# Performance work log

Measured on AMD Instinct MI355X. Metric: run time of the kernel, lower is better.

The kernel has to match this reference:

```python
import jax, jax.numpy as jnp
import numpy as np

H = 12      # num_attention_heads
D = 768     # hidden_size
DK = D // H # per-head dim


def setup_inputs() -> dict:
    key = jax.random.key(0)
    ks = jax.random.split(key, 8)
    B, S = 2, 4096
    scale = 0.02
    return {
        "query": jax.random.normal(ks[0], (B, S, D), jnp.float32),
        "key": jax.random.normal(ks[1], (B, S, D), jnp.float32),
        "value": jax.random.normal(ks[2], (B, S, D), jnp.float32),
        "mask": jnp.ones((B, S), jnp.float32),
        "Wq": jax.random.normal(ks[3], (D, D), jnp.float32) * scale,
        "bq": jnp.zeros((D,), jnp.float32),
        "Wk": jax.random.normal(ks[4], (D, D), jnp.float32) * scale,
        "bk": jnp.zeros((D,), jnp.float32),
        "Wv": jax.random.normal(ks[5], (D, D), jnp.float32) * scale,
        "bv": jnp.zeros((D,), jnp.float32),
    }


def reference(query, key, value, mask, Wq, bq, Wk, bk, Wv, bv):
    B, Sq, _ = query.shape
    Sk = key.shape[1]
    # attention mask: ones[B,Sq,1] * mask[B,1,Sk] -> [B,Sq,Sk] -> [B,1,Sq,Sk]
    attn_mask = jnp.ones((B, Sq, 1), jnp.float32) * mask[:, None, :]
    adder = (1.0 - attn_mask)[:, None, :, :] * -10000.0

    q = (query @ Wq + bq).reshape(B, Sq, H, DK).transpose(0, 2, 1, 3)  # [B,H,Sq,DK]
    k = (key @ Wk + bk).reshape(B, Sk, H, DK).transpose(0, 2, 1, 3)
    v = (value @ Wv + bv).reshape(B, Sk, H, DK).transpose(0, 2, 1, 3)

    scores = jnp.einsum("bhqd,bhkd->bhqk", q, k) / jnp.sqrt(jnp.float32(DK))
    scores = scores + adder
    probs = jax.nn.softmax(scores, axis=-1)  # dropout inactive (training=False)
    out = jnp.einsum("bhqk,bhkd->bhqd", probs, v)
    return out.transpose(0, 2, 1, 3).reshape(B, Sq, D)
```

## Files before the change

kernel.cpp:

```cpp
#include <hip/hip_runtime.h>
#include <stdint.h>

#define NH 12
#define DMODEL 768
#define HDK 64
#define SEQ 4096
#define NB 2

typedef __attribute__((ext_vector_type(8))) short bf16x8;
typedef __attribute__((ext_vector_type(4))) short s16x4;
typedef __attribute__((ext_vector_type(4))) float f32x4;
typedef __attribute__((ext_vector_type(16))) float f32x16;

#define LOG2E 1.44269504f
#define QSCALE 0.18033688f
#define CSUB 4.0f

__device__ __forceinline__ unsigned short f2bf(float x) {
    union { float f; unsigned u; } v; v.f = x;
    unsigned r = v.u + 0x7FFFu + ((v.u >> 16) & 1u);
    return (unsigned short)(r >> 16);
}

__device__ __forceinline__ unsigned pack2bf(float a, float b) {
    union { float f; unsigned u; } x, y; x.f = a; y.f = b;
    return __builtin_amdgcn_perm(y.u + 0x8000u, x.u + 0x8000u, 0x07060302u);
}

__device__ __forceinline__ unsigned pack2bf_t(float a, float b) {
    union { float f; unsigned u; } x, y; x.f = a; y.f = b;
    return __builtin_amdgcn_perm(y.u, x.u, 0x07060302u);
}

__device__ __forceinline__ void lds_dma16(const void* g, void* l) {
    __builtin_amdgcn_global_load_lds(
        (const __attribute__((address_space(1))) void*)g,
        (__attribute__((address_space(3))) void*)l, 16, 0, 0);
}

__global__ __launch_bounds__(256) void wt_kernel(
    const float* __restrict__ Wq, const float* __restrict__ Wk,
    const float* __restrict__ Wv, unsigned short* __restrict__ Wt) {
    __shared__ float ts[32][33];
    int mat = blockIdx.z;
    const float* W = (mat == 0) ? Wq : ((mat == 1) ? Wk : Wv);
    unsigned short* out = Wt + (size_t)mat * DMODEL * DMODEL;
    int k0 = blockIdx.x * 32;
    int n0 = blockIdx.y * 32;
    int t = threadIdx.x;
    int row = t >> 3, c4 = (t & 7) * 4;
    float4 v = *(const float4*)&W[(size_t)(k0 + row) * DMODEL + n0 + c4];
    ts[row][c4 + 0] = v.x; ts[row][c4 + 1] = v.y;
    ts[row][c4 + 2] = v.z; ts[row][c4 + 3] = v.w;
    __syncthreads();
    s16x4 o;
    o[0] = (short)f2bf(ts[c4 + 0][row]);
    o[1] = (short)f2bf(ts[c4 + 1][row]);
    o[2] = (short)f2bf(ts[c4 + 2][row]);
    o[3] = (short)f2bf(ts[c4 + 3][row]);
    *(s16x4*)&out[(size_t)(n0 + row) * DMODEL + k0 + c4] = o;
}

__global__ __launch_bounds__(256) void abf_kernel(
    const float* __restrict__ Aq, const float* __restrict__ Ak,
    const float* __restrict__ Av, unsigned short* __restrict__ Abf) {
    int mat = blockIdx.y;
    const float* A = (mat == 0) ? Aq : ((mat == 1) ? Ak : Av);
    unsigned short* o = Abf + (size_t)mat * NB * SEQ * DMODEL;
    int t = blockIdx.x * 256 + threadIdx.x;
    #pragma unroll
    for (int i = 0; i < 4; ++i) {
        size_t e = ((size_t)i * 196608 + t) * 8;
        float4 lo = *(const float4*)&A[e];
        float4 hi = *(const float4*)&A[e + 4];
        uint4 r;
        r.x = pack2bf(lo.x, lo.y); r.y = pack2bf(lo.z, lo.w);
        r.z = pack2bf(hi.x, hi.y); r.w = pack2bf(hi.z, hi.w);
        *(uint4*)&o[e] = r;
    }
}

__global__ __launch_bounds__(256) void qkv_gemm6(
    const unsigned short* __restrict__ Abf, const unsigned short* __restrict__ Wt,
    const float* __restrict__ bq, const float* __restrict__ bk,
    const float* __restrict__ bv,
    unsigned short* __restrict__ Qw, unsigned short* __restrict__ Kw,
    unsigned short* __restrict__ Vt) {
    __shared__ unsigned short As[2][128 * 64];
    __shared__ unsigned short Bs[2][128 * 64];
    int lin = blockIdx.x;
    int swz = (lin & 7) * 144 + (lin >> 3);
    int mat = swz / 384;
    int rr = swz - mat * 384;
    int mblk = rr / 6;
    int nblk = rr - mblk * 6;
    const unsigned short* A = Abf + (size_t)mat * NB * SEQ * DMODEL;
    const unsigned short* W = Wt + (size_t)mat * DMODEL * DMODEL;
    const float* bias = (mat == 0) ? bq : ((mat == 1) ? bk : bv);
    int m0 = mblk * 128;
    int n0 = nblk * 128;
    int tid = threadIdx.x;
    int lane = tid & 63, wv = tid >> 6;
    int wm = (wv & 1) * 64, wn = (wv >> 1) * 64;
    int lm = lane & 15, quad = lane >> 4;

    const unsigned short* aS[4];
    const unsigned short* bS[4];
    #pragma unroll
    for (int i = 0; i < 4; ++i) {
        int g = i * 256 + tid;
        int R = g >> 3, S = g & 7, c = S ^ (R & 7);
        aS[i] = A + (size_t)(m0 + R) * DMODEL + c * 8;
        bS[i] = W + (size_t)(n0 + R) * DMODEL + c * 8;
    }

    f32x4 acc[4][4] = {};
    int sx = lm & 7;
    const bool swapC = (mat < 2);

    #pragma unroll
    for (int i = 0; i < 4; ++i) {
        lds_dma16(aS[i], &As[0][(i * 256 + wv * 64) * 8]);
        lds_dma16(bS[i], &Bs[0][(i * 256 + wv * 64) * 8]);
        aS[i] += 64; bS[i] += 64;
    }
    __syncthreads();

    for (int kt = 0; kt < 12; ++kt) {
        int cur = kt & 1;
        if (kt < 11) {
            #pragma unroll
            for (int i = 0; i < 4; ++i) {
                lds_dma16(aS[i], &As[cur ^ 1][(i * 256 + wv * 64) * 8]);
                lds_dma16(bS[i], &Bs[cur ^ 1][(i * 256 + wv * 64) * 8]);
                aS[i] += 64; bS[i] += 64;
            }
        }
        #pragma unroll
        for (int ks = 0; ks < 2; ++ks) {
            bf16x8 af[4], bfr[4];
            #pragma unroll
            for (int i = 0; i < 4; ++i)
                af[i] = *(const bf16x8*)&As[cur][(wm + i * 16 + lm) * 64 +
                                                (((ks * 4 + quad) ^ sx) << 3)];
            #pragma unroll
            for (int j = 0; j < 4; ++j)
                bfr[j] = *(const bf16x8*)&Bs[cur][(wn + j * 16 + lm) * 64 +
                                                 (((ks * 4 + quad) ^ sx) << 3)];
            if (swapC) {
                #pragma unroll
                for (int i = 0; i < 4; ++i)
                    #pragma unroll
                    for (int j = 0; j < 4; ++j)
                        acc[i][j] = __builtin_amdgcn_mfma_f32_16x16x32_bf16(
                            bfr[j], af[i], acc[i][j], 0, 0, 0);
            } else {
                #pragma unroll
                for (int i = 0; i < 4; ++i)
                    #pragma unroll
                    for (int j = 0; j < 4; ++j)
                        acc[i][j] = __builtin_amdgcn_mfma_f32_16x16x32_bf16(
                            af[i], bfr[j], acc[i][j], 0, 0, 0);
            }
        }
        __syncthreads();
    }
    if (swapC) {
        float sc = (mat == 0) ? QSCALE : 1.0f;
        unsigned short* outp = (mat == 0) ? Qw : Kw;
        #pragma unroll
        for (int j = 0; j < 4; ++j) {
            int nbase = n0 + wn + j * 16 + quad * 4;
            f32x4 bvv = *(const f32x4*)&bias[nbase];
            int h = nbase >> 6, dk = nbase & 63;
            #pragma unroll
            for (int i = 0; i < 4; ++i) {
                int s = m0 + wm + i * 16 + lm;
                int b = s >> 12, ss = s & 4095;
                s16x4 o;
                #pragma unroll
                for (int r = 0; r < 4; ++r)
                    o[r] = (short)f2bf((acc[i][j][r] + bvv[r]) * sc);
                *(s16x4*)&outp[((size_t)(b * NH + h) * SEQ + ss) * HDK + dk] = o;
            }
        }
    } else {
        #pragma unroll
        for (int j = 0; j < 4; ++j) {
            int n = n0 + wn + j * 16 + lm;
            float bvv = bias[n];
            int h = n >> 6, dk = n & 63;
            #pragma unroll
            for (int i = 0; i < 4; ++i) {
                int mg = m0 + wm + i * 16 + quad * 4;
                int b = mg >> 12, s = mg & 4095;
                s16x4 o;
                #pragma unroll
                for (int r = 0; r < 4; ++r) o[r] = (short)f2bf(acc[i][j][r] + bvv);
                *(s16x4*)&Vt[((size_t)(b * NH + h) * HDK + dk) * SEQ + s] = o;
            }
        }
    }
}

__global__ __launch_bounds__(256) void qkv_gemm4(
    const float* __restrict__ Aq, const float* __restrict__ Ak,
    const float* __restrict__ Av, const unsigned short* __restrict__ Wt,
    const float* __restrict__ bq, const float* __restrict__ bk,
    const float* __restrict__ bv,
    unsigned short* __restrict__ Qw, unsigned short* __restrict__ Kw,
    unsigned short* __restrict__ Vt) {
    __shared__ float As[128 * 64];
    __shared__ unsigned short Bs[128 * 64];
    int lin = blockIdx.x;
    int swz = (lin & 7) * 144 + (lin >> 3);
    int mat = swz / 384;
    int rr = swz - mat * 384;
    int mblk = rr / 6;
    int nblk = rr - mblk * 6;
    const float* A = (mat == 0) ? Aq : ((mat == 1) ? Ak : Av);
    const unsigned short* W = Wt + (size_t)mat * DMODEL * DMODEL;
    const float* bias = (mat == 0) ? bq : ((mat == 1) ? bk : bv);
    int m0 = mblk * 128;
    int n0 = nblk * 128;
    int tid = threadIdx.x;
    int lane = tid & 63, wv = tid >> 6;
    int wm = (wv & 1) * 64, wn = (wv >> 1) * 64;
    int lm = lane & 15, quad = lane >> 4;

    const float* aS[8];
    float* aD[8];
    #pragma unroll
    for (int i = 0; i < 8; ++i) {
        int g = i * 256 + tid;
        int R = g >> 4, S = g & 15, c = (S & 8) | ((S & 7) ^ (R & 7));
        aS[i] = A + (size_t)(m0 + R) * DMODEL + c * 4;
        aD[i] = &As[(i * 256 + wv * 64) * 4];
    }
    const unsigned short* bS[4];
    unsigned short* bD[4];
    #pragma unroll
    for (int i = 0; i < 4; ++i) {
        int g = i * 256 + tid;
        int R = g >> 3, S = g & 7, c = S ^ (R & 7);
        bS[i] = W + (size_t)(n0 + R) * DMODEL + c * 8;
        bD[i] = &Bs[(i * 256 + wv * 64) * 8];
    }

    f32x4 acc[4][4] = {};
    int sx = lm & 7;
    const bool swapC = (mat < 2);
    for (int kt = 0; kt < 12; ++kt) {
        __syncthreads();
        #pragma unroll
        for (int i = 0; i < 8; ++i) lds_dma16(aS[i], aD[i]);
        #pragma unroll
        for (int i = 0; i < 4; ++i) lds_dma16(bS[i], bD[i]);
        #pragma unroll
        for (int i = 0; i < 8; ++i) aS[i] += 64;
        #pragma unroll
        for (int i = 0; i < 4; ++i) bS[i] += 64;
        __syncthreads();
        #pragma unroll
        for (int ks = 0; ks < 2; ++ks) {
            bf16x8 af[4], bfr[4];
            #pragma unroll
            for (int i = 0; i < 4; ++i) {
                int r = wm + i * 16 + lm;
                int c0 = ks * 8 + quad * 2;
                int s0 = (c0 & 8) | ((c0 & 7) ^ sx);
                int s1 = (c0 & 8) | (((c0 + 1) & 7) ^ sx);
                f32x4 lo = *(const f32x4*)&As[r * 64 + s0 * 4];
                f32x4 hi = *(const f32x4*)&As[r * 64 + s1 * 4];
                unsigned* au = (unsigned*)&af[i];
                au[0] = pack2bf(lo[0], lo[1]);
                au[1] = pack2bf(lo[2], lo[3]);
                au[2] = pack2bf(hi[0], hi[1]);
                au[3] = pack2bf(hi[2], hi[3]);
            }
            #pragma unroll
            for (int j = 0; j < 4; ++j)
                bfr[j] = *(const bf16x8*)&Bs[(wn + j * 16 + lm) * 64 +
                                             (((ks * 4 + quad) ^ sx) << 3)];
            if (swapC) {
                #pragma unroll
                for (int i = 0; i < 4; ++i)
                    #pragma unroll
                    for (int j = 0; j < 4; ++j)
                        acc[i][j] = __builtin_amdgcn_mfma_f32_16x16x32_bf16(
                            bfr[j], af[i], acc[i][j], 0, 0, 0);
            } else {
                #pragma unroll
                for (int i = 0; i < 4; ++i)
                    #pragma unroll
                    for (int j = 0; j < 4; ++j)
                        acc[i][j] = __builtin_amdgcn_mfma_f32_16x16x32_bf16(
                            af[i], bfr[j], acc[i][j], 0, 0, 0);
            }
        }
    }
    if (swapC) {
        float sc = (mat == 0) ? QSCALE : 1.0f;
        unsigned short* outp = (mat == 0) ? Qw : Kw;
        #pragma unroll
        for (int j = 0; j < 4; ++j) {
            int nbase = n0 + wn + j * 16 + quad * 4;
            f32x4 bvv = *(const f32x4*)&bias[nbase];
            int h = nbase >> 6, dk = nbase & 63;
            #pragma unroll
            for (int i = 0; i < 4; ++i) {
                int s = m0 + wm + i * 16 + lm;
                int b = s >> 12, ss = s & 4095;
                s16x4 o;
                #pragma unroll
                for (int r = 0; r < 4; ++r)
                    o[r] = (short)f2bf((acc[i][j][r] + bvv[r]) * sc);
                *(s16x4*)&outp[((size_t)(b * NH + h) * SEQ + ss) * HDK + dk] = o;
            }
        }
    } else {
        #pragma unroll
        for (int j = 0; j < 4; ++j) {
            int n = n0 + wn + j * 16 + lm;
            float bvv = bias[n];
            int h = n >> 6, dk = n & 63;
            #pragma unroll
            for (int i = 0; i < 4; ++i) {
                int mg = m0 + wm + i * 16 + quad * 4;
                int b = mg >> 12, s = mg & 4095;
                s16x4 o;
                #pragma unroll
                for (int r = 0; r < 4; ++r) o[r] = (short)f2bf(acc[i][j][r] + bvv);
                *(s16x4*)&Vt[((size_t)(b * NH + h) * HDK + dk) * SEQ + s] = o;
            }
        }
    }
}

__global__ __launch_bounds__(256, 2) void attn_kernel(
    const unsigned short* __restrict__ Qw, const unsigned short* __restrict__ Kw,
    const unsigned short* __restrict__ Vt, const float* __restrict__ mask,
    float* __restrict__ out) {
    __shared__ __align__(16) char smem[66560];
    unsigned short* KsB = (unsigned short*)smem;
    unsigned short* VsB = (unsigned short*)(smem + 32768);
    float* addsB = (float*)(smem + 65536);

    int lin = blockIdx.x;
    int swz = (lin & 7) * 96 + (lin >> 3);
    int q0 = (swz & 31) * 128;
    int bh = swz >> 5;
    int b = bh / NH, h = bh % NH;
    const unsigned short* Qb = Qw + (size_t)bh * SEQ * HDK;
    const char* Kb8 = (const char*)(Kw + (size_t)bh * SEQ * HDK);
    const char* Vb8 = (const char*)(Vt + (size_t)bh * HDK * SEQ);
    const float* mb = mask + (size_t)b * SEQ;
    int tid = threadIdx.x;
    int lane = tid & 63, wv = tid >> 6;
    int qg = wv >> 1, kvh = wv & 1;
    int L31 = lane & 31, hh = lane >> 5;
    const int sx7 = L31 & 7;

    int qrow = q0 + qg * 64 + L31;
    bf16x8 qa[4], qbv[4];
    #pragma unroll
    for (int t = 0; t < 4; ++t) {
        qa[t] = *(const bf16x8*)&Qb[(size_t)qrow * HDK + t * 16 + hh * 8];
        qbv[t] = *(const bf16x8*)&Qb[(size_t)(qrow + 32) * HDK + t * 16 + hh * 8];
    }

    unsigned koff[4], voff[4];
    #pragma unroll
    for (int i = 0; i < 4; ++i) {
        int cc = wv * 4 + i;
        {
            int rho = cc * 8 + (lane >> 3);
            int blk = rho >> 5, c = (rho >> 3) & 3, hb = (rho >> 2) & 1, r2 = rho & 3;
            int kc = blk * 32 + (c & 1) * 16 + hb * 8 + (c >> 1) * 4 + r2;
            int ch = (lane & 7) ^ (rho & 7);
            koff[i] = (unsigned)((kc * HDK + ch * 8) * 2);
        }
        {
            int d = cc * 4 + (lane >> 4);
            int c = lane & 15;
            int ch = (c & 8) | ((c & 7) ^ (d & 7));
            voff[i] = (unsigned)((d * SEQ + ch * 8) * 2);
        }
    }

    int tm = tid & 127;
    float mnext;
    {
        if (tid < 128) {
            float m0v = mb[tm];
            addsB[tm] = ((1.0f - m0v) * -10000.0f - CSUB) * LOG2E;
        }
        mnext = mb[128 + tm];
    }
    #pragma unroll
    for (int i = 0; i < 4; ++i) {
        lds_dma16(Kb8 + koff[i], KsB + (wv * 4 + i) * 512);
        lds_dma16(Vb8 + voff[i], VsB + (wv * 4 + i) * 512);
    }
    __syncthreads();

    f32x16 Oa[2] = {}, Ob[2] = {};
    float lpa = 0.0f, lpb = 0.0f;
    const f32x16 kZero = {};
    const int b0 = kvh * 2;

    for (int kt = 0; kt < 32; ++kt) {
        int cur = kt & 1;
        const unsigned short* Kc = KsB + cur * 8192;
        const unsigned short* Vc = VsB + cur * 8192;
        const float* adc = addsB + cur * 128;
        if (kt < 31) {
            const char* Kt8 = Kb8 + (size_t)(kt + 1) * 16384;
            const char* Vt8 = Vb8 + (size_t)(kt + 1) * 256;
            unsigned short* kd = KsB + (cur ^ 1) * 8192;
            unsigned short* vd = VsB + (cur ^ 1) * 8192;
            #pragma unroll
            for (int i = 0; i < 4; ++i) {
                lds_dma16(Kt8 + koff[i], kd + (wv * 4 + i) * 512);
                lds_dma16(Vt8 + voff[i], vd + (wv * 4 + i) * 512);
            }
        }
        if (tid < 128)
            addsB[(cur ^ 1) * 128 + tm] =
                ((1.0f - mnext) * -10000.0f - CSUB) * LOG2E;
        int mi = (kt < 30) ? (kt + 2) * 128 + tm : tm;
        mnext = mb[mi];

        #pragma unroll
        for (int bi = 0; bi < 2; ++bi) {
            int blk = b0 + bi;
            f32x16 sa, sb;
            __builtin_amdgcn_s_setprio(1);
            {
                bf16x8 kf = *(const bf16x8*)&Kc[(blk * 32 + L31) * 64 +
                                                ((hh ^ sx7) << 3)];
                sa = __builtin_amdgcn_mfma_f32_32x32x16_bf16(kf, qa[0], kZero, 0, 0, 0);
                sb = __builtin_amdgcn_mfma_f32_32x32x16_bf16(kf, qbv[0], kZero, 0, 0, 0);
            }
            #pragma unroll
            for (int t = 1; t < 4; ++t) {
                bf16x8 kf = *(const bf16x8*)&Kc[(blk * 32 + L31) * 64 +
                                                (((2 * t + hh) ^ sx7) << 3)];
                sa = __builtin_amdgcn_mfma_f32_32x32x16_bf16(kf, qa[t], sa, 0, 0, 0);
                sb = __builtin_amdgcn_mfma_f32_32x32x16_bf16(kf, qbv[t], sb, 0, 0, 0);
            }
            __builtin_amdgcn_s_setprio(0);

            unsigned pkkA[2][4], pkkB[2][4];
            #pragma unroll
            for (int c2 = 0; c2 < 4; ++c2) {
                f32x4 adv = *(const f32x4*)&adc[blk * 32 + (c2 & 1) * 16 +
                                                (c2 >> 1) * 4 + hh * 8];
                float a0 = __builtin_amdgcn_exp2f(sa[c2 * 4 + 0] + adv[0]);
                float a1 = __builtin_amdgcn_exp2f(sa[c2 * 4 + 1] + adv[1]);
                float a2 = __builtin_amdgcn_exp2f(sa[c2 * 4 + 2] + adv[2]);
                float a3 = __builtin_amdgcn_exp2f(sa[c2 * 4 + 3] + adv[3]);
                lpa += (a0 + a1) + (a2 + a3);
                pkkA[c2 & 1][2 * (c2 >> 1) + 0] = pack2bf_t(a0, a1);
                pkkA[c2 & 1][2 * (c2 >> 1) + 1] = pack2bf_t(a2, a3);
                float b0v = __builtin_amdgcn_exp2f(sb[c2 * 4 + 0] + adv[0]);
                float b1v = __builtin_amdgcn_exp2f(sb[c2 * 4 + 1] + adv[1]);
                float b2v = __builtin_amdgcn_exp2f(sb[c2 * 4 + 2] + adv[2]);
                float b3v = __builtin_amdgcn_exp2f(sb[c2 * 4 + 3] + adv[3]);
                lpb += (b0v + b1v) + (b2v + b3v);
                pkkB[c2 & 1][2 * (c2 >> 1) + 0] = pack2bf_t(b0v, b1v);
                pkkB[c2 & 1][2 * (c2 >> 1) + 1] = pack2bf_t(b2v, b3v);
            }

            __builtin_amdgcn_s_setprio(1);
            #pragma unroll
            for (int kbi = 0; kbi < 2; ++kbi) {
                bf16x8 pfA, pfB;
                unsigned* pa = (unsigned*)&pfA;
                unsigned* pb = (unsigned*)&pfB;
                pa[0] = pkkA[kbi][0]; pa[1] = pkkA[kbi][1];
                pa[2] = pkkA[kbi][2]; pa[3] = pkkA[kbi][3];
                pb[0] = pkkB[kbi][0]; pb[1] = pkkB[kbi][1];
                pb[2] = pkkB[kbi][2]; pb[3] = pkkB[kbi][3];
                int kb = blk * 2 + kbi;
                #pragma unroll
                for (int dj = 0; dj < 2; ++dj) {
                    int c = kb * 2 + hh;
                    int slot = (c & 8) | ((c & 7) ^ (lane & 7));
                    bf16x8 vf = *(const bf16x8*)&Vc[(dj * 32 + L31) * 128 + slot * 8];
                    Oa[dj] = __builtin_amdgcn_mfma_f32_32x32x16_bf16(vf, pfA, Oa[dj], 0, 0, 0);
                    Ob[dj] = __builtin_amdgcn_mfma_f32_32x32x16_bf16(vf, pfB, Ob[dj], 0, 0, 0);
                }
            }
            __builtin_amdgcn_s_setprio(0);
        }
        __syncthreads();
    }

    lpa += __shfl_xor(lpa, 32);
    lpb += __shfl_xor(lpb, 32);

    float* fb = (float*)smem + qg * 4224;
    if (kvh == 0) {
        #pragma unroll
        for (int dj = 0; dj < 2; ++dj)
            #pragma unroll
            for (int e = 0; e < 16; ++e) {
                fb[(dj * 16 + e) * 64 + lane] = Oa[dj][e];
                fb[(32 + dj * 16 + e) * 64 + lane] = Ob[dj][e];
            }
        fb[4096 + lane] = lpa;
        fb[4160 + lane] = lpb;
    }
    __syncthreads();
    if (kvh == 1) {
        #pragma unroll
        for (int dj = 0; dj < 2; ++dj)
            #pragma unroll
            for (int e = 0; e < 16; ++e) {
                Oa[dj][e] += fb[(dj * 16 + e) * 64 + lane];
                Ob[dj][e] += fb[(32 + dj * 16 + e) * 64 + lane];
            }
        float rla = 1.0f / (lpa + fb[4096 + lane]);
        float rlb = 1.0f / (lpb + fb[4160 + lane]);
        size_t basea = ((size_t)b * SEQ + qrow) * DMODEL + h * HDK;
        #pragma unroll
        for (int dj = 0; dj < 2; ++dj)
            #pragma unroll
            for (int c2 = 0; c2 < 4; ++c2) {
                int d = dj * 32 + 8 * c2 + 4 * hh;
                float4 o;
                o.x = Oa[dj][c2 * 4 + 0] * rla;
                o.y = Oa[dj][c2 * 4 + 1] * rla;
                o.z = Oa[dj][c2 * 4 + 2] * rla;
                o.w = Oa[dj][c2 * 4 + 3] * rla;
                *(float4*)&out[basea + d] = o;
                float4 o2;
                o2.x = Ob[dj][c2 * 4 + 0] * rlb;
                o2.y = Ob[dj][c2 * 4 + 1] * rlb;
                o2.z = Ob[dj][c2 * 4 + 2] * rlb;
                o2.w = Ob[dj][c2 * 4 + 3] * rlb;
                *(float4*)&out[basea + (size_t)32 * DMODEL + d] = o2;
            }
    }
}

extern "C" void kernel_launch(void* const* d_in, const int* in_sizes, int n_in,
                              void* d_out, int out_size, void* d_ws, size_t ws_size,
                              hipStream_t stream) {
    (void)in_sizes; (void)n_in; (void)out_size;
    const float* query = (const float*)d_in[0];
    const float* key   = (const float*)d_in[1];
    const float* value = (const float*)d_in[2];
    const float* mask  = (const float*)d_in[3];
    const float* Wq    = (const float*)d_in[4];
    const float* bq    = (const float*)d_in[5];
    const float* Wk    = (const float*)d_in[6];
    const float* bk    = (const float*)d_in[7];
    const float* Wv    = (const float*)d_in[8];
    const float* bv    = (const float*)d_in[9];

    const size_t WT_BYTES  = (size_t)3 * DMODEL * DMODEL * 2;
    const size_t ABF_BYTES = (size_t)3 * NB * SEQ * DMODEL * 2;
    const size_t QKV_BYTES = (size_t)NB * NH * SEQ * HDK * 2;

    unsigned short* Wt = (unsigned short*)d_ws;
    if (ws_size >= WT_BYTES + ABF_BYTES + 3 * QKV_BYTES) {
        unsigned short* Abf = (unsigned short*)((char*)d_ws + WT_BYTES);
        unsigned short* Qw = (unsigned short*)((char*)d_ws + WT_BYTES + ABF_BYTES);
        unsigned short* Kw = (unsigned short*)((char*)d_ws + WT_BYTES + ABF_BYTES + QKV_BYTES);
        unsigned short* Vt = (unsigned short*)((char*)d_ws + WT_BYTES + ABF_BYTES + 2 * QKV_BYTES);
        wt_kernel<<<dim3(24, 24, 3), 256, 0, stream>>>(Wq, Wk, Wv, Wt);
        abf_kernel<<<dim3(768, 3), 256, 0, stream>>>(query, key, value, Abf);
        qkv_gemm6<<<dim3(1152), 256, 0, stream>>>(Abf, Wt, bq, bk, bv, Qw, Kw, Vt);
        attn_kernel<<<dim3(768), 256, 0, stream>>>(Qw, Kw, Vt, mask, (float*)d_out);
    } else {
        unsigned short* Qw = (unsigned short*)((char*)d_ws + WT_BYTES);
        unsigned short* Kw = (unsigned short*)((char*)d_ws + WT_BYTES + QKV_BYTES);
        unsigned short* Vt = (unsigned short*)((char*)d_ws + WT_BYTES + 2 * QKV_BYTES);
        wt_kernel<<<dim3(24, 24, 3), 256, 0, stream>>>(Wq, Wk, Wv, Wt);
        qkv_gemm4<<<dim3(1152), 256, 0, stream>>>(query, key, value, Wt,
                                                  bq, bk, bv, Qw, Kw, Vt);
        attn_kernel<<<dim3(768), 256, 0, stream>>>(Qw, Kw, Vt, mask, (float*)d_out);
    }
}
```

Baseline: 305.7 us.

## Halve LDS tiles in QKV GEMM and attention to raise occupancy

The QKV projection GEMM now stages K-tiles of 32 instead of 64 (24 iterations), with a new 4-chunk swizzle and explicit vmcnt/lgkmcnt waits around raw barriers, and launch bounds of 4 blocks per CU. The attention kernel processes 64-key tiles instead of 128 (64 iterations), with halved shared memory and matching K/V swizzles, also targeting 4 blocks per CU. The aim is more resident waves to hide memory and exp latency, at the cost of twice as many barriers and iterations and a tighter register budget that may cause spills.

```diff
diff --git a/kernel.cpp b/kernel.cpp
--- a/kernel.cpp
+++ b/kernel.cpp
@@ -80,14 +80,14 @@
     }
 }
 
-__global__ __launch_bounds__(256) void qkv_gemm6(
+__global__ __launch_bounds__(256, 4) void qkv_gemm7(
     const unsigned short* __restrict__ Abf, const unsigned short* __restrict__ Wt,
     const float* __restrict__ bq, const float* __restrict__ bk,
     const float* __restrict__ bv,
     unsigned short* __restrict__ Qw, unsigned short* __restrict__ Kw,
     unsigned short* __restrict__ Vt) {
-    __shared__ unsigned short As[2][128 * 64];
-    __shared__ unsigned short Bs[2][128 * 64];
+    __shared__ unsigned short As[2][128 * 32];
+    __shared__ unsigned short Bs[2][128 * 32];
     int lin = blockIdx.x;
     int swz = (lin & 7) * 144 + (lin >> 3);
     int mat = swz / 384;
@@ -104,67 +104,70 @@
     int wm = (wv & 1) * 64, wn = (wv >> 1) * 64;
     int lm = lane & 15, quad = lane >> 4;
 
-    const unsigned short* aS[4];
-    const unsigned short* bS[4];
-    #pragma unroll
-    for (int i = 0; i < 4; ++i) {
+    const unsigned short* aS[2];
+    const unsigned short* bS[2];
+    #pragma unroll
+    for (int i = 0; i < 2; ++i) {
         int g = i * 256 + tid;
-        int R = g >> 3, S = g & 7, c = S ^ (R & 7);
-        aS[i] = A + (size_t)(m0 + R) * DMODEL + c * 8;
-        bS[i] = W + (size_t)(n0 + R) * DMODEL + c * 8;
+        int R = g >> 2, c = g & 3, ch = c ^ (R & 3);
+        aS[i] = A + (size_t)(m0 + R) * DMODEL + ch * 8;
+        bS[i] = W + (size_t)(n0 + R) * DMODEL + ch * 8;
     }
 
     f32x4 acc[4][4] = {};
-    int sx = lm & 7;
+    const int sx3 = lm & 3;
     const bool swapC = (mat < 2);
 
     #pragma unroll
-    for (int i = 0; i < 4; ++i) {
+    for (int i = 0; i < 2; ++i) {
         lds_dma16(aS[i], &As[0][(i * 256 + wv * 64) * 8]);
         lds_dma16(bS[i], &Bs[0][(i * 256 + wv * 64) * 8]);
-        aS[i] += 64; bS[i] += 64;
-    }
-    __syncthreads();
-
-    for (int kt = 0; kt < 12; ++kt) {
+        aS[i] += 32; bS[i] += 32;
+    }
+
+    for (int kt = 0; kt < 24; ++kt) {
         int cur = kt & 1;
-        if (kt < 11) {
-            #pragma unroll
-            for (int i = 0; i < 4; ++i) {
+        if (kt < 23) {
+            #pragma unroll
+            for (int i = 0; i < 2; ++i) {
                 lds_dma16(aS[i], &As[cur ^ 1][(i * 256 + wv * 64) * 8]);
                 lds_dma16(bS[i], &Bs[cur ^ 1][(i * 256 + wv * 64) * 8]);
-                aS[i] += 64; bS[i] += 64;
-            }
-        }
-        #pragma unroll
-        for (int ks = 0; ks < 2; ++ks) {
-            bf16x8 af[4], bfr[4];
+                aS[i] += 32; bS[i] += 32;
+            }
+            asm volatile("s_waitcnt vmcnt(4)" ::: "memory");
+        } else {
+            asm volatile("s_waitcnt vmcnt(0)" ::: "memory");
+        }
+        __builtin_amdgcn_s_barrier();
+
+        bf16x8 af[4], bfr[4];
+        #pragma unroll
+        for (int i = 0; i < 4; ++i)
+            af[i] = *(const bf16x8*)&As[cur][(wm + i * 16 + lm) * 32 +
+                                            ((quad ^ sx3) << 3)];
+        #pragma unroll
+        for (int j = 0; j < 4; ++j)
+            bfr[j] = *(const bf16x8*)&Bs[cur][(wn + j * 16 + lm) * 32 +
+                                             ((quad ^ sx3) << 3)];
+        if (swapC) {
             #pragma unroll
             for (int i = 0; i < 4; ++i)
-                af[i] = *(const bf16x8*)&As[cur][(wm + i * 16 + lm) * 64 +
-                                                (((ks * 4 + quad) ^ sx) << 3)];
-            #pragma unroll
-            for (int j = 0; j < 4; ++j)
-                bfr[j] = *(const bf16x8*)&Bs[cur][(wn + j * 16 + lm) * 64 +
-                                                 (((ks * 4 + quad) ^ sx) << 3)];
-            if (swapC) {
-                #pragma unroll
-                for (int i = 0; i < 4; ++i)
-                    #pragma unroll
-                    for (int j = 0; j < 4; ++j)
-                        acc[i][j] = __builtin_amdgcn_mfma_f32_16x16x32_bf16(
-                            bfr[j], af[i], acc[i][j], 0, 0, 0);
-            } else {
-                #pragma unroll
-                for (int i = 0; i < 4; ++i)
-                    #pragma unroll
-                    for (int j = 0; j < 4; ++j)
-                        acc[i][j] = __builtin_amdgcn_mfma_f32_16x16x32_bf16(
-                            af[i], bfr[j], acc[i][j], 0, 0, 0);
-            }
-        }
-        __syncthreads();
-    }
+                #pragma unroll
+                for (int j = 0; j < 4; ++j)
+                    acc[i][j] = __builtin_amdgcn_mfma_f32_16x16x32_bf16(
+                        bfr[j], af[i], acc[i][j], 0, 0, 0);
+        } else {
+            #pragma unroll
+            for (int i = 0; i < 4; ++i)
+                #pragma unroll
+                for (int j = 0; j < 4; ++j)
+                    acc[i][j] = __builtin_amdgcn_mfma_f32_16x16x32_bf16(
+                        af[i], bfr[j], acc[i][j], 0, 0, 0);
+        }
+        asm volatile("s_waitcnt lgkmcnt(0)" ::: "memory");
+        __builtin_amdgcn_s_barrier();
+    }
+
     if (swapC) {
         float sc = (mat == 0) ? QSCALE : 1.0f;
         unsigned short* outp = (mat == 0) ? Qw : Kw;
@@ -337,14 +340,14 @@
     }
 }
 
-__global__ __launch_bounds__(256, 2) void attn_kernel(
+__global__ __launch_bounds__(256, 4) void attn_kernel(
     const unsigned short* __restrict__ Qw, const unsigned short* __restrict__ Kw,
     const unsigned short* __restrict__ Vt, const float* __restrict__ mask,
     float* __restrict__ out) {
-    __shared__ __align__(16) char smem[66560];
+    __shared__ __align__(16) char smem[33792];
     unsigned short* KsB = (unsigned short*)smem;
-    unsigned short* VsB = (unsigned short*)(smem + 32768);
-    float* addsB = (float*)(smem + 65536);
+    unsigned short* VsB = (unsigned short*)(smem + 16384);
+    float* addsB = (float*)(smem + 32768);
 
     int lin = blockIdx.x;
     int swz = (lin & 7) * 96 + (lin >> 3);
@@ -369,10 +372,10 @@
         qbv[t] = *(const bf16x8*)&Qb[(size_t)(qrow + 32) * HDK + t * 16 + hh * 8];
     }
 
-    unsigned koff[4], voff[4];
-    #pragma unroll
-    for (int i = 0; i < 4; ++i) {
-        int cc = wv * 4 + i;
+    unsigned koff[2], voff[2];
+    #pragma unroll
+    for (int i = 0; i < 2; ++i) {
+        int cc = wv * 2 + i;
         {
             int rho = cc * 8 + (lane >> 3);
             int blk = rho >> 5, c = (rho >> 3) & 3, hb = (rho >> 2) & 1, r2 = rho & 3;
@@ -381,119 +384,112 @@
             koff[i] = (unsigned)((kc * HDK + ch * 8) * 2);
         }
         {
-            int d = cc * 4 + (lane >> 4);
-            int c = lane & 15;
-            int ch = (c & 8) | ((c & 7) ^ (d & 7));
+            int d = cc * 8 + (lane >> 3);
+            int c = lane & 7;
+            int ch = c ^ (d & 7);
             voff[i] = (unsigned)((d * SEQ + ch * 8) * 2);
         }
     }
 
-    int tm = tid & 127;
-    float mnext;
-    {
-        if (tid < 128) {
-            float m0v = mb[tm];
-            addsB[tm] = ((1.0f - m0v) * -10000.0f - CSUB) * LOG2E;
-        }
-        mnext = mb[128 + tm];
-    }
-    #pragma unroll
-    for (int i = 0; i < 4; ++i) {
-        lds_dma16(Kb8 + koff[i], KsB + (wv * 4 + i) * 512);
-        lds_dma16(Vb8 + voff[i], VsB + (wv * 4 + i) * 512);
+    float mnext = 0.0f;
+    if (tid < 64) {
+        addsB[tid] = ((1.0f - mb[tid]) * -10000.0f - CSUB) * LOG2E;
+        mnext = mb[64 + tid];
+    }
+    #pragma unroll
+    for (int i = 0; i < 2; ++i) {
+        lds_dma16(Kb8 + koff[i], KsB + (wv * 2 + i) * 512);
+        lds_dma16(Vb8 + voff[i], VsB + (wv * 2 + i) * 512);
     }
     __syncthreads();
 
     f32x16 Oa[2] = {}, Ob[2] = {};
     float lpa = 0.0f, lpb = 0.0f;
     const f32x16 kZero = {};
-    const int b0 = kvh * 2;
-
-    for (int kt = 0; kt < 32; ++kt) {
+    const int blk = kvh;
+
+    for (int kt = 0; kt < 64; ++kt) {
         int cur = kt & 1;
-        const unsigned short* Kc = KsB + cur * 8192;
-        const unsigned short* Vc = VsB + cur * 8192;
-        const float* adc = addsB + cur * 128;
-        if (kt < 31) {
-            const char* Kt8 = Kb8 + (size_t)(kt + 1) * 16384;
-            const char* Vt8 = Vb8 + (size_t)(kt + 1) * 256;
-            unsigned short* kd = KsB + (cur ^ 1) * 8192;
-            unsigned short* vd = VsB + (cur ^ 1) * 8192;
-            #pragma unroll
-            for (int i = 0; i < 4; ++i) {
-                lds_dma16(Kt8 + koff[i], kd + (wv * 4 + i) * 512);
-                lds_dma16(Vt8 + voff[i], vd + (wv * 4 + i) * 512);
-            }
-        }
-        if (tid < 128)
-            addsB[(cur ^ 1) * 128 + tm] =
+        const unsigned short* Kc = KsB + cur * 4096;
+        const unsigned short* Vc = VsB + cur * 4096;
+        const float* adc = addsB + cur * 64;
+        if (kt < 63) {
+            const char* Kt8 = Kb8 + (size_t)(kt + 1) * 8192;
+            const char* Vt8 = Vb8 + (size_t)(kt + 1) * 128;
+            unsigned short* kd = KsB + (cur ^ 1) * 4096;
+            unsigned short* vd = VsB + (cur ^ 1) * 4096;
+            #pragma unroll
+            for (int i = 0; i < 2; ++i) {
+                lds_dma16(Kt8 + koff[i], kd + (wv * 2 + i) * 512);
+                lds_dma16(Vt8 + voff[i], vd + (wv * 2 + i) * 512);
+            }
+        }
+        if (tid < 64) {
+            addsB[(cur ^ 1) * 64 + tid] =
                 ((1.0f - mnext) * -10000.0f - CSUB) * LOG2E;
-        int mi = (kt < 30) ? (kt + 2) * 128 + tm : tm;
-        mnext = mb[mi];
-
-        #pragma unroll
-        for (int bi = 0; bi < 2; ++bi) {
-            int blk = b0 + bi;
-            f32x16 sa, sb;
-            __builtin_amdgcn_s_setprio(1);
-            {
-                bf16x8 kf = *(const bf16x8*)&Kc[(blk * 32 + L31) * 64 +
-                                                ((hh ^ sx7) << 3)];
-                sa = __builtin_amdgcn_mfma_f32_32x32x16_bf16(kf, qa[0], kZero, 0, 0, 0);
-                sb = __builtin_amdgcn_mfma_f32_32x32x16_bf16(kf, qbv[0], kZero, 0, 0, 0);
-            }
-            #pragma unroll
-            for (int t = 1; t < 4; ++t) {
-                bf16x8 kf = *(const bf16x8*)&Kc[(blk * 32 + L31) * 64 +
-                                                (((2 * t + hh) ^ sx7) << 3)];
-                sa = __builtin_amdgcn_mfma_f32_32x32x16_bf16(kf, qa[t], sa, 0, 0, 0);
-                sb = __builtin_amdgcn_mfma_f32_32x32x16_bf16(kf, qbv[t], sb, 0, 0, 0);
-            }
-            __builtin_amdgcn_s_setprio(0);
-
-            unsigned pkkA[2][4], pkkB[2][4];
-            #pragma unroll
-            for (int c2 = 0; c2 < 4; ++c2) {
-                f32x4 adv = *(const f32x4*)&adc[blk * 32 + (c2 & 1) * 16 +
-                                                (c2 >> 1) * 4 + hh * 8];
-                float a0 = __builtin_amdgcn_exp2f(sa[c2 * 4 + 0] + adv[0]);
-                float a1 = __builtin_amdgcn_exp2f(sa[c2 * 4 + 1] + adv[1]);
-                float a2 = __builtin_amdgcn_exp2f(sa[c2 * 4 + 2] + adv[2]);
-                float a3 = __builtin_amdgcn_exp2f(sa[c2 * 4 + 3] + adv[3]);
-                lpa += (a0 + a1) + (a2 + a3);
-                pkkA[c2 & 1][2 * (c2 >> 1) + 0] = pack2bf_t(a0, a1);
-                pkkA[c2 & 1][2 * (c2 >> 1) + 1] = pack2bf_t(a2, a3);
-                float b0v = __builtin_amdgcn_exp2f(sb[c2 * 4 + 0] + adv[0]);
-                float b1v = __builtin_amdgcn_exp2f(sb[c2 * 4 + 1] + adv[1]);
-                float b2v = __builtin_amdgcn_exp2f(sb[c2 * 4 + 2] + adv[2]);
-                float b3v = __builtin_amdgcn_exp2f(sb[c2 * 4 + 3] + adv[3]);
-                lpb += (b0v + b1v) + (b2v + b3v);
-                pkkB[c2 & 1][2 * (c2 >> 1) + 0] = pack2bf_t(b0v, b1v);
-                pkkB[c2 & 1][2 * (c2 >> 1) + 1] = pack2bf_t(b2v, b3v);
-            }
-
-            __builtin_amdgcn_s_setprio(1);
-            #pragma unroll
-            for (int kbi = 0; kbi < 2; ++kbi) {
-                bf16x8 pfA, pfB;
-                unsigned* pa = (unsigned*)&pfA;
-                unsigned* pb = (unsigned*)&pfB;
-                pa[0] = pkkA[kbi][0]; pa[1] = pkkA[kbi][1];
-                pa[2] = pkkA[kbi][2]; pa[3] = pkkA[kbi][3];
-                pb[0] = pkkB[kbi][0]; pb[1] = pkkB[kbi][1];
-                pb[2] = pkkB[kbi][2]; pb[3] = pkkB[kbi][3];
-                int kb = blk * 2 + kbi;
-                #pragma unroll
-                for (int dj = 0; dj < 2; ++dj) {
-                    int c = kb * 2 + hh;
-                    int slot = (c & 8) | ((c & 7) ^ (lane & 7));
-                    bf16x8 vf = *(const bf16x8*)&Vc[(dj * 32 + L31) * 128 + slot * 8];
-                    Oa[dj] = __builtin_amdgcn_mfma_f32_32x32x16_bf16(vf, pfA, Oa[dj], 0, 0, 0);
-                    Ob[dj] = __builtin_amdgcn_mfma_f32_32x32x16_bf16(vf, pfB, Ob[dj], 0, 0, 0);
-                }
-            }
-            __builtin_amdgcn_s_setprio(0);
-        }
+            int mi = (kt < 62) ? (kt + 2) * 64 + tid : tid;
+            mnext = mb[mi];
+        }
+
+        f32x16 sa, sb;
+        __builtin_amdgcn_s_setprio(1);
+        {
+            bf16x8 kf = *(const bf16x8*)&Kc[(blk * 32 + L31) * 64 +
+                                            ((hh ^ sx7) << 3)];
+            sa = __builtin_amdgcn_mfma_f32_32x32x16_bf16(kf, qa[0], kZero, 0, 0, 0);
+            sb = __builtin_amdgcn_mfma_f32_32x32x16_bf16(kf, qbv[0], kZero, 0, 0, 0);
+        }
+        #pragma unroll
+        for (int t = 1; t < 4; ++t) {
+            bf16x8 kf = *(const bf16x8*)&Kc[(blk * 32 + L31) * 64 +
+                                            (((2 * t + hh) ^ sx7) << 3)];
+            sa = __builtin_amdgcn_mfma_f32_32x32x16_bf16(kf, qa[t], sa, 0, 0, 0);
+            sb = __builtin_amdgcn_mfma_f32_32x32x16_bf16(kf, qbv[t], sb, 0, 0, 0);
+        }
+        __builtin_amdgcn_s_setprio(0);
+
+        unsigned pkkA[2][4], pkkB[2][4];
+        #pragma unroll
+        for (int c2 = 0; c2 < 4; ++c2) {
+            f32x4 adv = *(const f32x4*)&adc[blk * 32 + (c2 & 1) * 16 +
+                                            (c2 >> 1) * 4 + hh * 8];
+            float a0 = __builtin_amdgcn_exp2f(sa[c2 * 4 + 0] + adv[0]);
+            float a1 = __builtin_amdgcn_exp2f(sa[c2 * 4 + 1] + adv[1]);
+            float a2 = __builtin_amdgcn_exp2f(sa[c2 * 4 + 2] + adv[2]);
+            float a3 = __builtin_amdgcn_exp2f(sa[c2 * 4 + 3] + adv[3]);
+            lpa += (a0 + a1) + (a2 + a3);
+            pkkA[c2 & 1][2 * (c2 >> 1) + 0] = pack2bf_t(a0, a1);
+            pkkA[c2 & 1][2 * (c2 >> 1) + 1] = pack2bf_t(a2, a3);
+            float b0v = __builtin_amdgcn_exp2f(sb[c2 * 4 + 0] + adv[0]);
+            float b1v = __builtin_amdgcn_exp2f(sb[c2 * 4 + 1] + adv[1]);
+            float b2v = __builtin_amdgcn_exp2f(sb[c2 * 4 + 2] + adv[2]);
+            float b3v = __builtin_amdgcn_exp2f(sb[c2 * 4 + 3] + adv[3]);
+            lpb += (b0v + b1v) + (b2v + b3v);
+            pkkB[c2 & 1][2 * (c2 >> 1) + 0] = pack2bf_t(b0v, b1v);
+            pkkB[c2 & 1][2 * (c2 >> 1) + 1] = pack2bf_t(b2v, b3v);
+        }
+
+        __builtin_amdgcn_s_setprio(1);
+        #pragma unroll
+        for (int kbi = 0; kbi < 2; ++kbi) {
+            bf16x8 pfA, pfB;
+            unsigned* pa = (unsigned*)&pfA;
+            unsigned* pb = (unsigned*)&pfB;
+            pa[0] = pkkA[kbi][0]; pa[1] = pkkA[kbi][1];
+            pa[2] = pkkA[kbi][2]; pa[3] = pkkA[kbi][3];
+            pb[0] = pkkB[kbi][0]; pb[1] = pkkB[kbi][1];
+            pb[2] = pkkB[kbi][2]; pb[3] = pkkB[kbi][3];
+            int kb = blk * 2 + kbi;
+            #pragma unroll
+            for (int dj = 0; dj < 2; ++dj) {
+                int c = kb * 2 + hh;
+                int slot = c ^ (lane & 7);
+                bf16x8 vf = *(const bf16x8*)&Vc[(dj * 32 + L31) * 64 + slot * 8];
+                Oa[dj] = __builtin_amdgcn_mfma_f32_32x32x16_bf16(vf, pfA, Oa[dj], 0, 0, 0);
+                Ob[dj] = __builtin_amdgcn_mfma_f32_32x32x16_bf16(vf, pfB, Ob[dj], 0, 0, 0);
+            }
+        }
+        __builtin_amdgcn_s_setprio(0);
         __syncthreads();
     }
 
@@ -572,7 +568,7 @@
         unsigned short* Vt = (unsigned short*)((char*)d_ws + WT_BYTES + ABF_BYTES + 2 * QKV_BYTES);
         wt_kernel<<<dim3(24, 24, 3), 256, 0, stream>>>(Wq, Wk, Wv, Wt);
         abf_kernel<<<dim3(768, 3), 256, 0, stream>>>(query, key, value, Abf);
-        qkv_gemm6<<<dim3(1152), 256, 0, stream>>>(Abf, Wt, bq, bk, bv, Qw, Kw, Vt);
+        qkv_gemm7<<<dim3(1152), 256, 0, stream>>>(Abf, Wt, bq, bk, bv, Qw, Kw, Vt);
         attn_kernel<<<dim3(768), 256, 0, stream>>>(Qw, Kw, Vt, mask, (float*)d_out);
     } else {
         unsigned short* Qw = (unsigned short*)((char*)d_ws + WT_BYTES);
```

Result: slower. 746.1 us (+144.1%).
